# Optimization experiments

Measured on AMD Instinct MI355X. Metric: run time of the kernel, lower is better.

## Reference

```python
import jax, jax.numpy as jnp
import numpy as np

B, S, D = 2, 256, 768
NUM_SPANS = 3
PROJ_DIM = 128


def _span_indices(seq_len):
    # (i, j) pairs exactly as the original double loop enumerates them;
    # span_idx fills slots 0..N-1 of the zero-initialized buffer sequentially.
    si, ei = [], []
    for i in range(seq_len):
        for j in range(i, min(seq_len, i + NUM_SPANS)):
            si.append(i)
            ei.append(j)
    return np.asarray(si, np.int32), np.asarray(ei, np.int32)


def setup_inputs() -> dict:
    key = jax.random.key(0)
    ks = jax.random.split(key, 6)
    sc = 0.02
    return {
        "hidden": jax.random.normal(ks[0], (B, S, D), jnp.float32),
        "width_emb": jax.random.normal(ks[1], (NUM_SPANS, D), jnp.float32) * sc,
        "w_span": jax.random.normal(ks[2], (3 * D, D), jnp.float32) * sc,
        "b_span": jnp.zeros((D,), jnp.float32),
        "w_cls": jax.random.normal(ks[3], (D, 1), jnp.float32) * sc,
        "b_cls": jnp.zeros((1,), jnp.float32),
        "w_p1": jax.random.normal(ks[4], (D, D), jnp.float32) * sc,
        "b_p1": jnp.zeros((D,), jnp.float32),
        "w_p2": jax.random.normal(ks[5], (D, PROJ_DIM), jnp.float32) * sc,
        "b_p2": jnp.zeros((PROJ_DIM,), jnp.float32),
    }


def reference(hidden, width_emb, w_span, b_span, w_cls, b_cls, w_p1, b_p1, w_p2, b_p2):
    Bv, Sv, Dv = hidden.shape
    total = Sv * (Sv + 1) // 2  # size of the zero-padded span buffer
    si, ei = _span_indices(Sv)
    n_valid = si.shape[0]  # 3*S - 3 actually-filled spans

    start = hidden[:, si]                      # [B, N, D] fused gather
    end = hidden[:, ei]                        # [B, N, D]
    w = width_emb[ei - si]                     # [N, D] width-embed lookup
    valid = jnp.concatenate(
        [start, end, jnp.broadcast_to(w[None], (Bv, n_valid, Dv))], axis=-1
    )  # [B, N, 3D]
    pad = jnp.zeros((Bv, total - n_valid, 3 * Dv), hidden.dtype)
    span_vecs = jnp.concatenate([valid, pad], axis=1)  # [B, total, 3D]

    span = span_vecs @ w_span + b_span          # span_rep: [B, total, D]
    logits = (span @ w_cls + b_cls)[..., 0]     # classifier: [B, total]
    proj = jax.nn.relu(span @ w_p1 + b_p1) @ w_p2 + b_p2  # [B, total, 128]
    return logits, proj
```

## Files before the change

kernel.cpp:

```cpp
#include <hip/hip_runtime.h>


typedef unsigned short u16;
typedef __attribute__((ext_vector_type(8))) short bf16x8;
typedef __attribute__((ext_vector_type(8))) unsigned short u16x8;
typedef __attribute__((ext_vector_type(4))) float f32x4;

#define D 768
#define S 256
#define TOTAL 32896
#define NVALID 765
#define NPADROW (TOTAL - NVALID)
#define PD 128
#define LOGITS_SZ (2 * TOTAL)
#define MROWS 1088

#define WS_P1   0
#define WS_TPAD 835584
#define WS_L    836352
#define WS_LW   837376
#define WS_LPAD 837379
#define WS_PPAD 837380
#define US_BYTE_OFF (837632 * 4)
#define US_HH  0
#define US_HL  835584
#define US_AH  1671168
#define US_AL  2064384
#define US_B1H 2457600
#define US_B1L 3637248
#define US_W1H 4816896
#define US_W1L 5406720

__device__ __forceinline__ u16 f2bf(float v) {
    unsigned u = __float_as_uint(v);
    u += 0x7fffu + ((u >> 16) & 1u);
    return (u16)(u >> 16);
}
__device__ __forceinline__ float bf2f(u16 h) {
    return __uint_as_float(((unsigned)h) << 16);
}

__device__ __forceinline__ void span_iw(int k, int& i, int& w) {
    if (k < 762)      { i = k / 3;  w = k - i * 3; }
    else if (k < 764) { i = 254;    w = k - 762; }
    else              { i = 255;    w = 0; }
}

__global__ __launch_bounds__(256) void k_prep(const float* __restrict__ hidden,
                                              const float* __restrict__ width_emb,
                                              const float* __restrict__ w_span,
                                              const float* __restrict__ b_span,
                                              const float* __restrict__ w_cls,
                                              const float* __restrict__ b_cls,
                                              const float* __restrict__ w_p1,
                                              const float* __restrict__ b_p1,
                                              float* __restrict__ ws) {
    u16* us = (u16*)((char*)ws + US_BYTE_OFF);
    const int bid = blockIdx.x, tid = threadIdx.x;
    __shared__ u16 Th[64][72];
    __shared__ u16 Tl[64][72];
    __shared__ float red[256];

    if (bid < 192) {
        const int e0 = bid * 2048 + tid * 8;
        float4 v0 = *(const float4*)&hidden[e0];
        float4 v1 = *(const float4*)&hidden[e0 + 4];
        float f[8] = {v0.x, v0.y, v0.z, v0.w, v1.x, v1.y, v1.z, v1.w};
        u16x8 h, l;
        #pragma unroll
        for (int c = 0; c < 8; ++c) {
            u16 hh = f2bf(f[c]);
            h[c] = hh;
            l[c] = f2bf(f[c] - bf2f(hh));
        }
        *(u16x8*)&us[US_AH + e0] = h;
        *(u16x8*)&us[US_AL + e0] = l;
        return;
    }
    const float* tsrc = nullptr;
    u16 *tdh = nullptr, *tdl = nullptr;
    int kb = 0, nb = 0;
    if (bid < 480) {
        int t2 = bid - 192;
        int g = t2 / 144, rem = t2 % 144;
        kb = rem / 12; nb = rem % 12;
        tsrc = w_span + (size_t)g * D * D;
        tdh = us + US_B1H + (size_t)g * D * D;
        tdl = us + US_B1L + (size_t)g * D * D;
    } else if (bid < 624) {
        int t3 = bid - 480;
        kb = t3 / 12; nb = t3 % 12;
        tsrc = w_p1;
        tdh = us + US_W1H;
        tdl = us + US_W1L;
    }
    if (tsrc) {
        #pragma unroll
        for (int r4 = 0; r4 < 4; ++r4) {
            const int srow = r4 * 16 + (tid >> 4);
            const int scol = (tid & 15) * 4;
            float4 v = *(const float4*)&tsrc[(size_t)(kb * 64 + srow) * D + nb * 64 + scol];
            float f[4] = {v.x, v.y, v.z, v.w};
            #pragma unroll
            for (int c = 0; c < 4; ++c) {
                u16 hh = f2bf(f[c]);
                Th[scol + c][srow] = hh;
                Tl[scol + c][srow] = f2bf(f[c] - bf2f(hh));
            }
        }
        __syncthreads();
        const int orow = tid >> 2, kp = (tid & 3) * 16;
        const size_t didx = (size_t)(nb * 64 + orow) * D + kb * 64 + kp;
        *(u16x8*)&tdh[didx]     = *(const u16x8*)&Th[orow][kp];
        *(u16x8*)&tdh[didx + 8] = *(const u16x8*)&Th[orow][kp + 8];
        *(u16x8*)&tdl[didx]     = *(const u16x8*)&Tl[orow][kp];
        *(u16x8*)&tdl[didx + 8] = *(const u16x8*)&Tl[orow][kp + 8];
        return;
    }
    const int dl = tid & 63, kc = tid >> 6;
    if (bid < 660) {
        const int t4 = bid - 624;
        const int w = t4 / 12, seg = t4 % 12;
        const int d = seg * 64 + dl;
        const float* Aw = w_span + (size_t)(2 * D) * D;
        const float* we = width_emb + w * D;
        float p = 0.f;
        #pragma unroll 4
        for (int k = kc * 192; k < kc * 192 + 192; ++k)
            p = fmaf(we[k], Aw[(size_t)k * D + d], p);
        red[tid] = p; __syncthreads();
        if (kc == 0) {
            float v = red[dl] + red[64 + dl] + red[128 + dl] + red[192 + dl] + b_span[d];
            u16 hh = f2bf(v);
            const size_t idx = (size_t)(1024 + w) * D + d;
            us[US_HH + idx] = hh;
            us[US_HL + idx] = f2bf(v - bf2f(hh));
        }
    } else if (bid < 672) {
        const int d = (bid - 660) * 64 + dl;
        float p = 0.f;
        #pragma unroll 4
        for (int k = kc * 192; k < kc * 192 + 192; ++k)
            p = fmaf(b_span[k], w_p1[(size_t)k * D + d], p);
        red[tid] = p; __syncthreads();
        if (kc == 0) {
            float v = red[dl] + red[64 + dl] + red[128 + dl] + red[192 + dl] + b_p1[d];
            ws[WS_TPAD + d] = fmaxf(v, 0.f);
        }
    } else {
        if (tid < 64) {
            float a = 0.f;
            #pragma unroll
            for (int i = 0; i < 12; ++i) a = fmaf(b_span[tid + 64 * i], w_cls[tid + 64 * i], a);
            for (int off = 32; off > 0; off >>= 1) a += __shfl_down(a, off, 64);
            if (tid == 0) ws[WS_LPAD] = a + b_cls[0];
        }
    }
}

#define MFMA(A, B, C) __builtin_amdgcn_mfma_f32_16x16x32_bf16(A, B, C, 0, 0, 0)
#define LD8(P) (*(const bf16x8*)(P))

__global__ __launch_bounds__(256) void k_g1(float* __restrict__ ws) {
    u16* us = (u16*)((char*)ws + US_BYTE_OFF);
    const int wid = blockIdx.x * 4 + (threadIdx.x >> 6);
    const int lane = threadIdx.x & 63;
    const int mt = wid & 31, nt = wid >> 5;
    const int m0 = mt * 16, n0 = nt * 32;
    const int lr = lane & 15, lk8 = (lane >> 4) * 8;
    const u16* Ah = us + US_AH; const u16* Al = us + US_AL;
    const u16* Bh = us + US_B1H; const u16* Bl = us + US_B1L;
    const size_t aoff = (size_t)(m0 + lr) * D + lk8;
    const size_t b0 = (size_t)(n0 + lr) * D + lk8;
    const size_t b1 = b0 + (size_t)16 * D;
    f32x4 acc0 = {0,0,0,0}, acc1 = {0,0,0,0};
    bf16x8 ah = LD8(Ah + aoff), al = LD8(Al + aoff);
    bf16x8 bh0 = LD8(Bh + b0), bl0 = LD8(Bl + b0);
    bf16x8 bh1 = LD8(Bh + b1), bl1 = LD8(Bl + b1);
    for (int kt = 0; kt < 24; ++kt) {
        bf16x8 cah = ah, cal = al, cbh0 = bh0, cbl0 = bl0, cbh1 = bh1, cbl1 = bl1;
        if (kt < 23) {
            const size_t o = (size_t)(kt + 1) * 32;
            ah = LD8(Ah + aoff + o); al = LD8(Al + aoff + o);
            bh0 = LD8(Bh + b0 + o);  bl0 = LD8(Bl + b0 + o);
            bh1 = LD8(Bh + b1 + o);  bl1 = LD8(Bl + b1 + o);
        }
        acc0 = MFMA(cah, cbh0, acc0);
        acc0 = MFMA(cah, cbl0, acc0);
        acc0 = MFMA(cal, cbh0, acc0);
        acc1 = MFMA(cah, cbh1, acc1);
        acc1 = MFMA(cah, cbl1, acc1);
        acc1 = MFMA(cal, cbh1, acc1);
    }
    const int g = (n0 >= D);
    const int cb = n0 - g * D;
    const int row0 = g * 512 + m0 + (lane >> 4) * 4;
    u16* Hh = us + US_HH; u16* Hl = us + US_HL;
    #pragma unroll
    for (int r = 0; r < 4; ++r) {
        const size_t base = (size_t)(row0 + r) * D;
        float v0 = acc0[r], v1 = acc1[r];
        u16 h0 = f2bf(v0), h1 = f2bf(v1);
        Hh[base + cb + lr] = h0;       Hl[base + cb + lr] = f2bf(v0 - bf2f(h0));
        Hh[base + cb + 16 + lr] = h1;  Hl[base + cb + 16 + lr] = f2bf(v1 - bf2f(h1));
    }
}

__global__ __launch_bounds__(256) void k_g2(const float* __restrict__ w_cls,
                                            const float* __restrict__ b_cls,
                                            const float* __restrict__ w_p2,
                                            const float* __restrict__ b_p2,
                                            float* __restrict__ ws) {
    u16* us = (u16*)((char*)ws + US_BYTE_OFF);
    const int bid = blockIdx.x, tid = threadIdx.x;
    const u16* Hh = us + US_HH; const u16* Hl = us + US_HL;
    if (bid < 390) {
        const int wid = bid * 4 + (tid >> 6);
        const int lane = tid & 63;
        const int mt = wid % 65, nt = wid / 65;
        const int m0 = mt * 16, n0 = nt * 32;
        const int lr = lane & 15, lk8 = (lane >> 4) * 8;
        const u16* Bh = us + US_W1H; const u16* Bl = us + US_W1L;
        const size_t aoff = (size_t)(m0 + lr) * D + lk8;
        const size_t b0 = (size_t)(n0 + lr) * D + lk8;
        const size_t b1 = b0 + (size_t)16 * D;
        f32x4 acc0 = {0,0,0,0}, acc1 = {0,0,0,0};
        bf16x8 ah = LD8(Hh + aoff), al = LD8(Hl + aoff);
        bf16x8 bh0 = LD8(Bh + b0), bl0 = LD8(Bl + b0);
        bf16x8 bh1 = LD8(Bh + b1), bl1 = LD8(Bl + b1);
        for (int kt = 0; kt < 24; ++kt) {
            bf16x8 cah = ah, cal = al, cbh0 = bh0, cbl0 = bl0, cbh1 = bh1, cbl1 = bl1;
            if (kt < 23) {
                const size_t o = (size_t)(kt + 1) * 32;
                ah = LD8(Hh + aoff + o); al = LD8(Hl + aoff + o);
                bh0 = LD8(Bh + b0 + o);  bl0 = LD8(Bl + b0 + o);
                bh1 = LD8(Bh + b1 + o);  bl1 = LD8(Bl + b1 + o);
            }
            acc0 = MFMA(cah, cbh0, acc0);
            acc0 = MFMA(cah, cbl0, acc0);
            acc0 = MFMA(cal, cbh0, acc0);
            acc1 = MFMA(cah, cbh1, acc1);
            acc1 = MFMA(cah, cbl1, acc1);
            acc1 = MFMA(cal, cbh1, acc1);
        }
        float* P1 = ws + WS_P1;
        const int row0 = m0 + (lane >> 4) * 4;
        #pragma unroll
        for (int r = 0; r < 4; ++r) {
            const size_t base = (size_t)(row0 + r) * D;
            P1[base + n0 + lr] = acc0[r];
            P1[base + n0 + 16 + lr] = acc1[r];
        }
    } else if (bid < 422) {
        const int w64 = tid >> 6, lane = tid & 63;
        const int rbase = (bid - 390) * 32 + w64 * 8;
        for (int rr = 0; rr < 8; ++rr) {
            const int r = rbase + rr;
            const u16* hh = Hh + (size_t)r * D;
            const u16* hl = Hl + (size_t)r * D;
            float a = 0.f;
            #pragma unroll
            for (int i = 0; i < 12; ++i) {
                const int d = lane + 64 * i;
                a = fmaf(bf2f(hh[d]) + bf2f(hl[d]), w_cls[d], a);
            }
            for (int off = 32; off > 0; off >>= 1) a += __shfl_down(a, off, 64);
            if (lane == 0) ws[WS_L + r] = a;
        }
    } else if (bid == 422) {
        if (tid < 192) {
            const int w = tid >> 6, lane = tid & 63;
            const u16* hh = Hh + (size_t)(1024 + w) * D;
            const u16* hl = Hl + (size_t)(1024 + w) * D;
            float a = 0.f;
            #pragma unroll
            for (int i = 0; i < 12; ++i) {
                const int d = lane + 64 * i;
                a = fmaf(bf2f(hh[d]) + bf2f(hl[d]), w_cls[d], a);
            }
            for (int off = 32; off > 0; off >>= 1) a += __shfl_down(a, off, 64);
            if (lane == 0) ws[WS_LW + w] = a + b_cls[0];
        }
    } else {
        __shared__ float redp[128];
        const int j = tid & 127, h2 = tid >> 7;
        float acc = 0.f;
        #pragma unroll 4
        for (int it = 0; it < 384; ++it) {
            const int d = h2 * 384 + it;
            acc = fmaf(ws[WS_TPAD + d], w_p2[(size_t)d * PD + j], acc);
        }
        if (h2) redp[j] = acc;
        __syncthreads();
        if (!h2) ws[WS_PPAD + j] = acc + redp[j] + b_p2[j];
    }
}

__global__ __launch_bounds__(256) void k_stage3(const float* __restrict__ w_p2,
                                                const float* __restrict__ b_p1,
                                                const float* __restrict__ b_p2,
                                                const float* __restrict__ ws,
                                                float* __restrict__ out) {
    const int bid = blockIdx.x, tid = threadIdx.x;
    if (bid < 512) {
        const int t0 = bid * 256 + tid;
        if (t0 < 2 * NPADROW) {
            int b = t0 / NPADROW;
            out[b * TOTAL + NVALID + (t0 - b * NPADROW)] = ws[WS_LPAD];
        }
        const float4 pp = *(const float4*)&ws[WS_PPAD + ((tid & 31) << 2)];
        float4* out4 = (float4*)(out + LOGITS_SZ);
        const long long totalU = (long long)2 * NPADROW * 32;
        for (long long u = t0; u < totalU; u += 131072) {
            int rb = (int)(u >> 5);
            int b = rb / NPADROW;
            int kk = rb - b * NPADROW;
            out4[((size_t)b * TOTAL + NVALID + kk) * 32 + (int)(u & 31)] = pp;
        }
        return;
    }
    const int sb = bid - 512;
    __shared__ float tld[D * 2];
    __shared__ float red[2 * PD];
    const float* P1 = ws + WS_P1;
    {
        const int s = tid >> 7, dl = tid & 127;
        const int q = sb * 2 + s;
        const int b = q >= 765;
        const int k = q - 765 * b;
        int i, w; span_iw(k, i, w);
        const size_t rs = (size_t)(b * S + i) * D;
        const size_t re = (size_t)(512 + b * S + i + w) * D;
        const size_t rw = (size_t)(1024 + w) * D;
        #pragma unroll
        for (int p = 0; p < 6; ++p) {
            const int dd = dl + 128 * p;
            float val = P1[rs + dd] + P1[re + dd] + P1[rw + dd] + b_p1[dd];
            tld[dd * 2 + s] = fmaxf(val, 0.f);
        }
    }
    if (tid < 2) {
        const int q2 = sb * 2 + tid;
        const int b2 = q2 >= 765, k2 = q2 - 765 * b2;
        int i2, w2; span_iw(k2, i2, w2);
        out[b2 * TOTAL + k2] = ws[WS_L + b2 * S + i2]
                             + ws[WS_L + 512 + b2 * S + i2 + w2] + ws[WS_LW + w2];
    }
    __syncthreads();
    const int j = tid & 127, h = tid >> 7;
    float a0 = 0.f, a1 = 0.f;
    const float* wp = w_p2 + (size_t)h * 384 * PD + j;
    const float* tb = tld + h * 384 * 2;
    #pragma unroll 4
    for (int it = 0; it < 384; ++it) {
        const float wv = wp[(size_t)it * PD];
        a0 = fmaf(wv, tb[it * 2], a0);
        a1 = fmaf(wv, tb[it * 2 + 1], a1);
    }
    if (h) { red[j] = a0; red[PD + j] = a1; }
    __syncthreads();
    if (!h) {
        const float bp = b_p2[j];
        const float v[2] = {a0 + red[j] + bp, a1 + red[PD + j] + bp};
        #pragma unroll
        for (int s4 = 0; s4 < 2; ++s4) {
            const int q2 = sb * 2 + s4;
            const int b2 = q2 >= 765, k2 = q2 - 765 * b2;
            out[LOGITS_SZ + ((size_t)b2 * TOTAL + k2) * PD + j] = v[s4];
        }
    }
}

extern "C" void kernel_launch(void* const* d_in, const int* in_sizes, int n_in,
                              void* d_out, int out_size, void* d_ws, size_t ws_size,
                              hipStream_t stream) {
    const float* hidden    = (const float*)d_in[0];
    const float* width_emb = (const float*)d_in[1];
    const float* w_span    = (const float*)d_in[2];
    const float* b_span    = (const float*)d_in[3];
    const float* w_cls     = (const float*)d_in[4];
    const float* b_cls     = (const float*)d_in[5];
    const float* w_p1      = (const float*)d_in[6];
    const float* b_p1      = (const float*)d_in[7];
    const float* w_p2      = (const float*)d_in[8];
    const float* b_p2      = (const float*)d_in[9];
    float* out = (float*)d_out;
    float* ws  = (float*)d_ws;

    k_prep<<<673, 256, 0, stream>>>(hidden, width_emb, w_span, b_span, w_cls, b_cls,
                                    w_p1, b_p1, ws);
    k_g1<<<384, 256, 0, stream>>>(ws);
    k_g2<<<424, 256, 0, stream>>>(w_cls, b_cls, w_p2, b_p2, ws);
    k_stage3<<<1277, 256, 0, stream>>>(w_p2, b_p1, b_p2, ws, out);
}
```

Measured before the change: 202.4 us.

## Fold w_span into w_p1 weights and reassociate span projection GEMMs

Reassociates the computation so the start/end halves of w_span are first multiplied by w_p1 into a combined 768x1536 weight, and hidden is then multiplied by this fused weight once. Classifier logits come from hidden dotted with a precomputed w_span·w_cls vector, and the width-embedding contribution is precomputed through w_p1. This replaces two chained GEMMs over hidden with a weight-only GEMM plus one GEMM over hidden. The GEMM inner loop also gains a three-stage register prefetch. The cost is an extra weight-by-weight GEMM on every call and a different rounding path through the split-bf16 products.

Measured after the change: 202.3 us. Within noise of the previous version (-0.1%).

```diff
diff --git a/kernel.cpp b/kernel.cpp
--- a/kernel.cpp
+++ b/kernel.cpp
@@ -13,23 +13,25 @@
 #define NPADROW (TOTAL - NVALID)
 #define PD 128
 #define LOGITS_SZ (2 * TOTAL)
-#define MROWS 1088
 
 #define WS_P1   0
-#define WS_TPAD 835584
-#define WS_L    836352
-#define WS_LW   837376
-#define WS_LPAD 837379
-#define WS_PPAD 837380
-#define US_BYTE_OFF (837632 * 4)
-#define US_HH  0
-#define US_HL  835584
-#define US_AH  1671168
-#define US_AL  2064384
-#define US_B1H 2457600
-#define US_B1L 3637248
-#define US_W1H 4816896
-#define US_W1L 5406720
+#define WS_WE3  786432
+#define WS_TPAD 788736
+#define WS_CLS  789504
+#define WS_L    791040
+#define WS_LW   792064
+#define WS_LPAD 792067
+#define WS_PPAD 792068
+#define WS_P1W  792196
+#define US_BYTE_OFF (794624 * 4)
+#define US_AH   0
+#define US_AL   393216
+#define US_W1TH 786432
+#define US_W1TL 1376256
+#define US_BSH  1966080
+#define US_BSL  3145728
+#define US_GTH  4325376
+#define US_GTL  5505024
 
 __device__ __forceinline__ u16 f2bf(float v) {
     unsigned u = __float_as_uint(v);
@@ -39,67 +41,29 @@
 __device__ __forceinline__ float bf2f(u16 h) {
     return __uint_as_float(((unsigned)h) << 16);
 }
-
 __device__ __forceinline__ void span_iw(int k, int& i, int& w) {
     if (k < 762)      { i = k / 3;  w = k - i * 3; }
     else if (k < 764) { i = 254;    w = k - 762; }
     else              { i = 255;    w = 0; }
 }
 
-__global__ __launch_bounds__(256) void k_prep(const float* __restrict__ hidden,
-                                              const float* __restrict__ width_emb,
-                                              const float* __restrict__ w_span,
-                                              const float* __restrict__ b_span,
-                                              const float* __restrict__ w_cls,
-                                              const float* __restrict__ b_cls,
-                                              const float* __restrict__ w_p1,
-                                              const float* __restrict__ b_p1,
-                                              float* __restrict__ ws) {
+#define MFMA(A,B,C) __builtin_amdgcn_mfma_f32_16x16x32_bf16(A,B,C,0,0,0)
+#define LD8(P) (*(const bf16x8*)(P))
+
+__global__ __launch_bounds__(256) void k0(const float* __restrict__ w_span,
+                                          const float* __restrict__ w_p1,
+                                          float* __restrict__ ws) {
     u16* us = (u16*)((char*)ws + US_BYTE_OFF);
     const int bid = blockIdx.x, tid = threadIdx.x;
-    __shared__ u16 Th[64][72];
-    __shared__ u16 Tl[64][72];
-    __shared__ float red[256];
-
-    if (bid < 192) {
-        const int e0 = bid * 2048 + tid * 8;
-        float4 v0 = *(const float4*)&hidden[e0];
-        float4 v1 = *(const float4*)&hidden[e0 + 4];
-        float f[8] = {v0.x, v0.y, v0.z, v0.w, v1.x, v1.y, v1.z, v1.w};
-        u16x8 h, l;
-        #pragma unroll
-        for (int c = 0; c < 8; ++c) {
-            u16 hh = f2bf(f[c]);
-            h[c] = hh;
-            l[c] = f2bf(f[c] - bf2f(hh));
-        }
-        *(u16x8*)&us[US_AH + e0] = h;
-        *(u16x8*)&us[US_AL + e0] = l;
-        return;
-    }
-    const float* tsrc = nullptr;
-    u16 *tdh = nullptr, *tdl = nullptr;
-    int kb = 0, nb = 0;
-    if (bid < 480) {
-        int t2 = bid - 192;
-        int g = t2 / 144, rem = t2 % 144;
-        kb = rem / 12; nb = rem % 12;
-        tsrc = w_span + (size_t)g * D * D;
-        tdh = us + US_B1H + (size_t)g * D * D;
-        tdl = us + US_B1L + (size_t)g * D * D;
-    } else if (bid < 624) {
-        int t3 = bid - 480;
-        kb = t3 / 12; nb = t3 % 12;
-        tsrc = w_p1;
-        tdh = us + US_W1H;
-        tdl = us + US_W1L;
-    }
-    if (tsrc) {
+    if (bid < 144) {
+        __shared__ u16 Th[64][72];
+        __shared__ u16 Tl[64][72];
+        const int kb = bid / 12, nb = bid % 12;
         #pragma unroll
         for (int r4 = 0; r4 < 4; ++r4) {
             const int srow = r4 * 16 + (tid >> 4);
             const int scol = (tid & 15) * 4;
-            float4 v = *(const float4*)&tsrc[(size_t)(kb * 64 + srow) * D + nb * 64 + scol];
+            float4 v = *(const float4*)&w_p1[(size_t)(kb * 64 + srow) * D + nb * 64 + scol];
             float f[4] = {v.x, v.y, v.z, v.w};
             #pragma unroll
             for (int c = 0; c < 4; ++c) {
@@ -111,17 +75,115 @@
         __syncthreads();
         const int orow = tid >> 2, kp = (tid & 3) * 16;
         const size_t didx = (size_t)(nb * 64 + orow) * D + kb * 64 + kp;
-        *(u16x8*)&tdh[didx]     = *(const u16x8*)&Th[orow][kp];
-        *(u16x8*)&tdh[didx + 8] = *(const u16x8*)&Th[orow][kp + 8];
-        *(u16x8*)&tdl[didx]     = *(const u16x8*)&Tl[orow][kp];
-        *(u16x8*)&tdl[didx + 8] = *(const u16x8*)&Tl[orow][kp + 8];
-        return;
-    }
-    const int dl = tid & 63, kc = tid >> 6;
-    if (bid < 660) {
-        const int t4 = bid - 624;
-        const int w = t4 / 12, seg = t4 % 12;
-        const int d = seg * 64 + dl;
+        *(u16x8*)&us[US_W1TH + didx]     = *(const u16x8*)&Th[orow][kp];
+        *(u16x8*)&us[US_W1TH + didx + 8] = *(const u16x8*)&Th[orow][kp + 8];
+        *(u16x8*)&us[US_W1TL + didx]     = *(const u16x8*)&Tl[orow][kp];
+        *(u16x8*)&us[US_W1TL + didx + 8] = *(const u16x8*)&Tl[orow][kp + 8];
+    } else {
+        const int e0 = (bid - 144) * 2048 + tid * 8;
+        float4 v0 = *(const float4*)&w_span[e0];
+        float4 v1 = *(const float4*)&w_span[e0 + 4];
+        float f[8] = {v0.x, v0.y, v0.z, v0.w, v1.x, v1.y, v1.z, v1.w};
+        u16x8 h, l;
+        #pragma unroll
+        for (int c = 0; c < 8; ++c) {
+            u16 hh = f2bf(f[c]);
+            h[c] = hh;
+            l[c] = f2bf(f[c] - bf2f(hh));
+        }
+        *(u16x8*)&us[US_BSH + e0] = h;
+        *(u16x8*)&us[US_BSL + e0] = l;
+    }
+}
+
+#define DECLSETS \
+    bf16x8 aH0,aL0,b0H0,b0L0,b1H0,b1L0, aH1,aL1,b0H1,b0L1,b1H1,b1L1, aH2,aL2,b0H2,b0L2,b1H2,b1L2;
+#define LSET(Sn, KT) { const size_t o_ = (size_t)(KT) * 32; \
+    aH##Sn = LD8(pAh + o_); aL##Sn = LD8(pAl + o_); \
+    b0H##Sn = LD8(pB0h + o_); b0L##Sn = LD8(pB0l + o_); \
+    b1H##Sn = LD8(pB1h + o_); b1L##Sn = LD8(pB1l + o_); }
+#define MM6(Sn) { \
+    acc0 = MFMA(aH##Sn, b0H##Sn, acc0); acc0 = MFMA(aH##Sn, b0L##Sn, acc0); acc0 = MFMA(aL##Sn, b0H##Sn, acc0); \
+    acc1 = MFMA(aH##Sn, b1H##Sn, acc1); acc1 = MFMA(aH##Sn, b1L##Sn, acc1); acc1 = MFMA(aL##Sn, b1H##Sn, acc1); }
+
+__global__ __launch_bounds__(256) void kA(const float* __restrict__ hidden,
+                                          const float* __restrict__ width_emb,
+                                          const float* __restrict__ w_span,
+                                          const float* __restrict__ b_span,
+                                          const float* __restrict__ w_cls,
+                                          const float* __restrict__ b_cls,
+                                          const float* __restrict__ w_p1,
+                                          const float* __restrict__ b_p1,
+                                          float* __restrict__ ws) {
+    u16* us = (u16*)((char*)ws + US_BYTE_OFF);
+    const int bid = blockIdx.x, tid = threadIdx.x;
+    if (bid < 576) {
+        const int wid = bid * 4 + (tid >> 6);
+        const int lane = tid & 63;
+        const int g = wid >= 1152;
+        const int w2 = wid - g * 1152;
+        const int n0 = (w2 % 48) * 16, i0 = (w2 / 48) * 32;
+        const int lr = lane & 15, lk8 = (lane >> 4) * 8;
+        const u16* pAh = us + US_W1TH + (size_t)(n0 + lr) * D + lk8;
+        const u16* pAl = us + US_W1TL + (size_t)(n0 + lr) * D + lk8;
+        const u16* pB0h = us + US_BSH + (size_t)(g * D + i0 + lr) * D + lk8;
+        const u16* pB0l = us + US_BSL + (size_t)(g * D + i0 + lr) * D + lk8;
+        const u16* pB1h = pB0h + (size_t)16 * D;
+        const u16* pB1l = pB0l + (size_t)16 * D;
+        f32x4 acc0 = {0,0,0,0}, acc1 = {0,0,0,0};
+        DECLSETS
+        LSET(0, 0) LSET(1, 1) LSET(2, 2)
+        for (int kt = 0; kt < 24; kt += 3) {
+            MM6(0)
+            if (kt + 3 < 24) LSET(0, kt + 3)
+            MM6(1)
+            if (kt + 4 < 24) LSET(1, kt + 4)
+            MM6(2)
+            if (kt + 5 < 24) LSET(2, kt + 5)
+        }
+        const int nr0 = n0 + (lane >> 4) * 4;
+        #pragma unroll
+        for (int r = 0; r < 4; ++r) {
+            const size_t base = (size_t)(g * D + nr0 + r) * D + i0;
+            float v0 = acc0[r], v1 = acc1[r];
+            u16 h0 = f2bf(v0), h1 = f2bf(v1);
+            us[US_GTH + base + lr] = h0;      us[US_GTL + base + lr] = f2bf(v0 - bf2f(h0));
+            us[US_GTH + base + 16 + lr] = h1; us[US_GTL + base + 16 + lr] = f2bf(v1 - bf2f(h1));
+        }
+    } else if (bid < 768) {
+        const int e0 = (bid - 576) * 2048 + tid * 8;
+        float4 v0 = *(const float4*)&hidden[e0];
+        float4 v1 = *(const float4*)&hidden[e0 + 4];
+        float f[8] = {v0.x, v0.y, v0.z, v0.w, v1.x, v1.y, v1.z, v1.w};
+        u16x8 h, l;
+        #pragma unroll
+        for (int c = 0; c < 8; ++c) {
+            u16 hh = f2bf(f[c]);
+            h[c] = hh;
+            l[c] = f2bf(f[c] - bf2f(hh));
+        }
+        *(u16x8*)&us[US_AH + e0] = h;
+        *(u16x8*)&us[US_AL + e0] = l;
+    } else if (bid < 864) {
+        const int w64 = tid >> 6, lane = tid & 63;
+        #pragma unroll
+        for (int q = 0; q < 4; ++q) {
+            const int rr = (bid - 768) * 16 + w64 * 4 + q;
+            const float* row = w_span + (size_t)rr * D;
+            float a = 0.f;
+            #pragma unroll
+            for (int i = 0; i < 12; ++i) {
+                const int d = lane + 64 * i;
+                a = fmaf(row[d], w_cls[d], a);
+            }
+            for (int off = 32; off > 0; off >>= 1) a += __shfl_down(a, off, 64);
+            if (lane == 0) ws[WS_CLS + rr] = a;
+        }
+    } else if (bid < 900) {
+        __shared__ float red[256];
+        const int dl = tid & 63, kc = tid >> 6;
+        const int t4 = bid - 864;
+        const int w = t4 / 12, d = (t4 % 12) * 64 + dl;
         const float* Aw = w_span + (size_t)(2 * D) * D;
         const float* we = width_emb + w * D;
         float p = 0.f;
@@ -129,24 +191,19 @@
         for (int k = kc * 192; k < kc * 192 + 192; ++k)
             p = fmaf(we[k], Aw[(size_t)k * D + d], p);
         red[tid] = p; __syncthreads();
-        if (kc == 0) {
-            float v = red[dl] + red[64 + dl] + red[128 + dl] + red[192 + dl] + b_span[d];
-            u16 hh = f2bf(v);
-            const size_t idx = (size_t)(1024 + w) * D + d;
-            us[US_HH + idx] = hh;
-            us[US_HL + idx] = f2bf(v - bf2f(hh));
-        }
-    } else if (bid < 672) {
-        const int d = (bid - 660) * 64 + dl;
+        if (kc == 0)
+            ws[WS_WE3 + w * D + d] = red[dl] + red[64 + dl] + red[128 + dl] + red[192 + dl] + b_span[d];
+    } else if (bid < 912) {
+        __shared__ float red[256];
+        const int dl = tid & 63, kc = tid >> 6;
+        const int d = (bid - 900) * 64 + dl;
         float p = 0.f;
         #pragma unroll 4
         for (int k = kc * 192; k < kc * 192 + 192; ++k)
             p = fmaf(b_span[k], w_p1[(size_t)k * D + d], p);
         red[tid] = p; __syncthreads();
-        if (kc == 0) {
-            float v = red[dl] + red[64 + dl] + red[128 + dl] + red[192 + dl] + b_p1[d];
-            ws[WS_TPAD + d] = fmaxf(v, 0.f);
-        }
+        if (kc == 0)
+            ws[WS_TPAD + d] = fmaxf(red[dl] + red[64 + dl] + red[128 + dl] + red[192 + dl] + b_p1[d], 0.f);
     } else {
         if (tid < 64) {
             float a = 0.f;
@@ -158,125 +215,85 @@
     }
 }
 
-#define MFMA(A, B, C) __builtin_amdgcn_mfma_f32_16x16x32_bf16(A, B, C, 0, 0, 0)
-#define LD8(P) (*(const bf16x8*)(P))
-
-__global__ __launch_bounds__(256) void k_g1(float* __restrict__ ws) {
-    u16* us = (u16*)((char*)ws + US_BYTE_OFF);
-    const int wid = blockIdx.x * 4 + (threadIdx.x >> 6);
-    const int lane = threadIdx.x & 63;
-    const int mt = wid & 31, nt = wid >> 5;
-    const int m0 = mt * 16, n0 = nt * 32;
-    const int lr = lane & 15, lk8 = (lane >> 4) * 8;
-    const u16* Ah = us + US_AH; const u16* Al = us + US_AL;
-    const u16* Bh = us + US_B1H; const u16* Bl = us + US_B1L;
-    const size_t aoff = (size_t)(m0 + lr) * D + lk8;
-    const size_t b0 = (size_t)(n0 + lr) * D + lk8;
-    const size_t b1 = b0 + (size_t)16 * D;
-    f32x4 acc0 = {0,0,0,0}, acc1 = {0,0,0,0};
-    bf16x8 ah = LD8(Ah + aoff), al = LD8(Al + aoff);
-    bf16x8 bh0 = LD8(Bh + b0), bl0 = LD8(Bl + b0);
-    bf16x8 bh1 = LD8(Bh + b1), bl1 = LD8(Bl + b1);
-    for (int kt = 0; kt < 24; ++kt) {
-        bf16x8 cah = ah, cal = al, cbh0 = bh0, cbl0 = bl0, cbh1 = bh1, cbl1 = bl1;
-        if (kt < 23) {
-            const size_t o = (size_t)(kt + 1) * 32;
-            ah = LD8(Ah + aoff + o); al = LD8(Al + aoff + o);
-            bh0 = LD8(Bh + b0 + o);  bl0 = LD8(Bl + b0 + o);
-            bh1 = LD8(Bh + b1 + o);  bl1 = LD8(Bl + b1 + o);
-        }
-        acc0 = MFMA(cah, cbh0, acc0);
-        acc0 = MFMA(cah, cbl0, acc0);
-        acc0 = MFMA(cal, cbh0, acc0);
-        acc1 = MFMA(cah, cbh1, acc1);
-        acc1 = MFMA(cah, cbl1, acc1);
-        acc1 = MFMA(cal, cbh1, acc1);
-    }
-    const int g = (n0 >= D);
-    const int cb = n0 - g * D;
-    const int row0 = g * 512 + m0 + (lane >> 4) * 4;
-    u16* Hh = us + US_HH; u16* Hl = us + US_HL;
-    #pragma unroll
-    for (int r = 0; r < 4; ++r) {
-        const size_t base = (size_t)(row0 + r) * D;
-        float v0 = acc0[r], v1 = acc1[r];
-        u16 h0 = f2bf(v0), h1 = f2bf(v1);
-        Hh[base + cb + lr] = h0;       Hl[base + cb + lr] = f2bf(v0 - bf2f(h0));
-        Hh[base + cb + 16 + lr] = h1;  Hl[base + cb + 16 + lr] = f2bf(v1 - bf2f(h1));
-    }
-}
-
-__global__ __launch_bounds__(256) void k_g2(const float* __restrict__ w_cls,
-                                            const float* __restrict__ b_cls,
-                                            const float* __restrict__ w_p2,
-                                            const float* __restrict__ b_p2,
-                                            float* __restrict__ ws) {
+__global__ __launch_bounds__(256) void kB(const float* __restrict__ hidden,
+                                          const float* __restrict__ w_cls,
+                                          const float* __restrict__ b_cls,
+                                          const float* __restrict__ w_p1,
+                                          const float* __restrict__ b_p1,
+                                          const float* __restrict__ w_p2,
+                                          const float* __restrict__ b_p2,
+                                          float* __restrict__ ws) {
     u16* us = (u16*)((char*)ws + US_BYTE_OFF);
     const int bid = blockIdx.x, tid = threadIdx.x;
-    const u16* Hh = us + US_HH; const u16* Hl = us + US_HL;
-    if (bid < 390) {
+    if (bid < 384) {
         const int wid = bid * 4 + (tid >> 6);
         const int lane = tid & 63;
-        const int mt = wid % 65, nt = wid / 65;
-        const int m0 = mt * 16, n0 = nt * 32;
+        const int m0 = (wid & 31) * 16, n0 = (wid >> 5) * 32;
         const int lr = lane & 15, lk8 = (lane >> 4) * 8;
-        const u16* Bh = us + US_W1H; const u16* Bl = us + US_W1L;
-        const size_t aoff = (size_t)(m0 + lr) * D + lk8;
-        const size_t b0 = (size_t)(n0 + lr) * D + lk8;
-        const size_t b1 = b0 + (size_t)16 * D;
+        const u16* pAh = us + US_AH + (size_t)(m0 + lr) * D + lk8;
+        const u16* pAl = us + US_AL + (size_t)(m0 + lr) * D + lk8;
+        const u16* pB0h = us + US_GTH + (size_t)(n0 + lr) * D + lk8;
+        const u16* pB0l = us + US_GTL + (size_t)(n0 + lr) * D + lk8;
+        const u16* pB1h = pB0h + (size_t)16 * D;
+        const u16* pB1l = pB0l + (size_t)16 * D;
         f32x4 acc0 = {0,0,0,0}, acc1 = {0,0,0,0};
-        bf16x8 ah = LD8(Hh + aoff), al = LD8(Hl + aoff);
-        bf16x8 bh0 = LD8(Bh + b0), bl0 = LD8(Bl + b0);
-        bf16x8 bh1 = LD8(Bh + b1), bl1 = LD8(Bl + b1);
-        for (int kt = 0; kt < 24; ++kt) {
-            bf16x8 cah = ah, cal = al, cbh0 = bh0, cbl0 = bl0, cbh1 = bh1, cbl1 = bl1;
-            if (kt < 23) {
-                const size_t o = (size_t)(kt + 1) * 32;
-                ah = LD8(Hh + aoff + o); al = LD8(Hl + aoff + o);
-                bh0 = LD8(Bh + b0 + o);  bl0 = LD8(Bl + b0 + o);
-                bh1 = LD8(Bh + b1 + o);  bl1 = LD8(Bl + b1 + o);
-            }
-            acc0 = MFMA(cah, cbh0, acc0);
-            acc0 = MFMA(cah, cbl0, acc0);
-            acc0 = MFMA(cal, cbh0, acc0);
-            acc1 = MFMA(cah, cbh1, acc1);
-            acc1 = MFMA(cah, cbl1, acc1);
-            acc1 = MFMA(cal, cbh1, acc1);
+        DECLSETS
+        LSET(0, 0) LSET(1, 1) LSET(2, 2)
+        for (int kt = 0; kt < 24; kt += 3) {
+            MM6(0)
+            if (kt + 3 < 24) LSET(0, kt + 3)
+            MM6(1)
+            if (kt + 4 < 24) LSET(1, kt + 4)
+            MM6(2)
+            if (kt + 5 < 24) LSET(2, kt + 5)
         }
         float* P1 = ws + WS_P1;
-        const int row0 = m0 + (lane >> 4) * 4;
+        const int mr0 = m0 + (lane >> 4) * 4;
         #pragma unroll
         for (int r = 0; r < 4; ++r) {
-            const size_t base = (size_t)(row0 + r) * D;
-            P1[base + n0 + lr] = acc0[r];
-            P1[base + n0 + 16 + lr] = acc1[r];
-        }
-    } else if (bid < 422) {
+            const size_t base = (size_t)(mr0 + r) * 1536 + n0;
+            P1[base + lr] = acc0[r];
+            P1[base + 16 + lr] = acc1[r];
+        }
+    } else if (bid < 416) {
         const int w64 = tid >> 6, lane = tid & 63;
-        const int rbase = (bid - 390) * 32 + w64 * 8;
-        for (int rr = 0; rr < 8; ++rr) {
-            const int r = rbase + rr;
-            const u16* hh = Hh + (size_t)r * D;
-            const u16* hl = Hl + (size_t)r * D;
+        const int rbase = (bid - 384) * 32 + w64 * 8;
+        for (int rr2 = 0; rr2 < 8; ++rr2) {
+            const int rr = rbase + rr2;
+            const int g = rr >= 512, r = rr & 511;
+            const float* hr = hidden + (size_t)r * D;
+            const float* cl = ws + WS_CLS + g * D;
             float a = 0.f;
             #pragma unroll
             for (int i = 0; i < 12; ++i) {
                 const int d = lane + 64 * i;
-                a = fmaf(bf2f(hh[d]) + bf2f(hl[d]), w_cls[d], a);
+                a = fmaf(hr[d], cl[d], a);
             }
             for (int off = 32; off > 0; off >>= 1) a += __shfl_down(a, off, 64);
-            if (lane == 0) ws[WS_L + r] = a;
-        }
-    } else if (bid == 422) {
+            if (lane == 0) ws[WS_L + rr] = a;
+        }
+    } else if (bid < 452) {
+        __shared__ float red[256];
+        const int dl = tid & 63, kc = tid >> 6;
+        const int t4 = bid - 416;
+        const int w = t4 / 12, d = (t4 % 12) * 64 + dl;
+        const float* we = ws + WS_WE3 + w * D;
+        float p = 0.f;
+        #pragma unroll 4
+        for (int k = kc * 192; k < kc * 192 + 192; ++k)
+            p = fmaf(we[k], w_p1[(size_t)k * D + d], p);
+        red[tid] = p; __syncthreads();
+        if (kc == 0)
+            ws[WS_P1W + w * D + d] = red[dl] + red[64 + dl] + red[128 + dl] + red[192 + dl] + b_p1[d];
+    } else if (bid == 452) {
         if (tid < 192) {
             const int w = tid >> 6, lane = tid & 63;
-            const u16* hh = Hh + (size_t)(1024 + w) * D;
-            const u16* hl = Hl + (size_t)(1024 + w) * D;
+            const float* we = ws + WS_WE3 + w * D;
             float a = 0.f;
             #pragma unroll
             for (int i = 0; i < 12; ++i) {
                 const int d = lane + 64 * i;
-                a = fmaf(bf2f(hh[d]) + bf2f(hl[d]), w_cls[d], a);
+                a = fmaf(we[d], w_cls[d], a);
             }
             for (int off = 32; off > 0; off >>= 1) a += __shfl_down(a, off, 64);
             if (lane == 0) ws[WS_LW + w] = a + b_cls[0];
@@ -296,11 +313,10 @@
     }
 }
 
-__global__ __launch_bounds__(256) void k_stage3(const float* __restrict__ w_p2,
-                                                const float* __restrict__ b_p1,
-                                                const float* __restrict__ b_p2,
-                                                const float* __restrict__ ws,
-                                                float* __restrict__ out) {
+__global__ __launch_bounds__(256) void kC(const float* __restrict__ w_p2,
+                                          const float* __restrict__ b_p2,
+                                          const float* __restrict__ ws,
+                                          float* __restrict__ out) {
     const int bid = blockIdx.x, tid = threadIdx.x;
     if (bid < 512) {
         const int t0 = bid * 256 + tid;
@@ -329,13 +345,13 @@
         const int b = q >= 765;
         const int k = q - 765 * b;
         int i, w; span_iw(k, i, w);
-        const size_t rs = (size_t)(b * S + i) * D;
-        const size_t re = (size_t)(512 + b * S + i + w) * D;
-        const size_t rw = (size_t)(1024 + w) * D;
+        const size_t rs = (size_t)(b * S + i) * 1536;
+        const size_t re = (size_t)(b * S + i + w) * 1536 + D;
+        const float* pw = ws + WS_P1W + w * D;
         #pragma unroll
         for (int p = 0; p < 6; ++p) {
             const int dd = dl + 128 * p;
-            float val = P1[rs + dd] + P1[re + dd] + P1[rw + dd] + b_p1[dd];
+            float val = P1[rs + dd] + P1[re + dd] + pw[dd];
             tld[dd * 2 + s] = fmaxf(val, 0.f);
         }
     }
@@ -387,9 +403,9 @@
     float* out = (float*)d_out;
     float* ws  = (float*)d_ws;
 
-    k_prep<<<673, 256, 0, stream>>>(hidden, width_emb, w_span, b_span, w_cls, b_cls,
-                                    w_p1, b_p1, ws);
-    k_g1<<<384, 256, 0, stream>>>(ws);
-    k_g2<<<424, 256, 0, stream>>>(w_cls, b_cls, w_p2, b_p2, ws);
-    k_stage3<<<1277, 256, 0, stream>>>(w_p2, b_p1, b_p2, ws, out);
-}
+    k0<<<720, 256, 0, stream>>>(w_span, w_p1, ws);
+    kA<<<913, 256, 0, stream>>>(hidden, width_emb, w_span, b_span, w_cls, b_cls,
+                                w_p1, b_p1, ws);
+    kB<<<454, 256, 0, stream>>>(hidden, w_cls, b_cls, w_p1, b_p1, w_p2, b_p2, ws);
+    kC<<<1277, 256, 0, stream>>>(w_p2, b_p2, ws, out);
+}
```
